# Kernel tuning notes

Hardware: AMD Instinct MI355X
Metric: run time of the kernel (lower is better)

## Reference

```python
import jax, jax.numpy as jnp
import numpy as np

B, H, W, C = 32, 64, 64, 512
NH, WIN, SHIFT = 16, 8, 4
S = WIN * WIN           # tokens per window = 64
HD = C // NH            # head dim = 32
FF = 4 * C
EPS = 1e-5
NW = (H // WIN) * (W // WIN)  # windows per image = 64


def _build_attn_mask():
    # Static shifted-window mask, same construction as SwinBlock_tp.__init__
    img = np.zeros((H, W), np.float32)
    slices = (slice(0, -WIN), slice(-WIN, -SHIFT), slice(-SHIFT, None))
    cnt = 0
    for hs in slices:
        for ws in slices:
            img[hs, ws] = cnt
            cnt += 1
    # window_partition on (1,H,W,1)
    m = img.reshape(H // WIN, WIN, W // WIN, WIN).transpose(0, 2, 1, 3).reshape(-1, S)
    diff = m[:, None, :] - m[:, :, None]            # (NW, S, S)
    return jnp.asarray(diff != 0)[:, None, :, :]     # (NW, 1, S, S) bool, True = masked

_ATTN_MASK = _build_attn_mask()


def _layernorm(x, g, b):
    mu = jnp.mean(x, axis=-1, keepdims=True)
    var = jnp.var(x, axis=-1, keepdims=True)
    return (x - mu) * jax.lax.rsqrt(var + EPS) * g + b


def _window_partition(x):
    # (B,H,W,C) -> (B*NW, S, C)
    x = x.reshape(B, H // WIN, WIN, W // WIN, WIN, C)
    x = x.transpose(0, 1, 3, 2, 4, 5)
    return x.reshape(-1, S, C)


def _window_reverse(x):
    # (B*NW, S, C) -> (B,H,W,C)
    x = x.reshape(B, H // WIN, W // WIN, WIN, WIN, C)
    x = x.transpose(0, 1, 3, 2, 4, 5)
    return x.reshape(B, H, W, C)


def setup_inputs() -> dict:
    key = jax.random.key(0)
    ks = jax.random.split(key, 8)
    sd = 0.02
    return {
        "hidden_states": jax.random.normal(ks[0], (B, H * W, C), jnp.float32),
        "Wqkv": jax.random.normal(ks[1], (C, 3 * C), jnp.float32) * sd,
        "bqkv": jnp.zeros((3 * C,), jnp.float32),
        "Wo": jax.random.normal(ks[2], (C, C), jnp.float32) * sd,
        "bo": jnp.zeros((C,), jnp.float32),
        "ln1_g": jnp.ones((C,), jnp.float32),
        "ln1_b": jnp.zeros((C,), jnp.float32),
        "ln2_g": jnp.ones((C,), jnp.float32),
        "ln2_b": jnp.zeros((C,), jnp.float32),
        "W1": jax.random.normal(ks[3], (C, FF), jnp.float32) * sd,
        "b1": jnp.zeros((FF,), jnp.float32),
        "W2": jax.random.normal(ks[4], (FF, C), jnp.float32) * sd,
        "b2": jnp.zeros((C,), jnp.float32),
    }


def reference(hidden_states, Wqkv, bqkv, Wo, bo, ln1_g, ln1_b, ln2_g, ln2_b, W1, b1, W2, b2):
    shortcut = hidden_states
    x = _layernorm(hidden_states, ln1_g, ln1_b).reshape(B, H, W, C)
    x = jnp.roll(x, shift=(-SHIFT, -SHIFT), axis=(1, 2))
    xw = _window_partition(x)                                  # (B*NW, S, C)

    qkv = xw @ Wqkv + bqkv                                     # (B*NW, S, 3C)
    q, k, v = jnp.split(qkv, 3, axis=-1)
    q = q.reshape(-1, S, NH, HD)
    k = k.reshape(-1, S, NH, HD)
    v = v.reshape(-1, S, NH, HD)
    scale = 1.0 / jnp.sqrt(jnp.float32(HD))
    scores = jnp.einsum("nqhd,nkhd->nhqk", q, k) * scale      # (B*NW, NH, S, S)
    mask = jnp.tile(_ATTN_MASK, (B, 1, 1, 1))                  # (B*NW, 1, S, S)
    scores = jnp.where(mask, -10000.0, scores)
    probs = jax.nn.softmax(scores, axis=-1)
    attn = jnp.einsum("nhqk,nkhd->nqhd", probs, v).reshape(-1, S, C)
    attn = attn @ Wo + bo                                      # out proj (+bias fused)

    x = _window_reverse(attn)
    x = jnp.roll(x, shift=(SHIFT, SHIFT), axis=(1, 2)).reshape(B, H * W, C)
    x = shortcut + x

    y = _layernorm(x, ln2_g, ln2_b)
    y = jax.nn.gelu(y @ W1 + b1, approximate=True) @ W2 + b2
    return x + y
```

## Files before the change

kernel.cpp:

```cpp
#include <hip/hip_runtime.h>
#include <hip/hip_bf16.h>
#include <math.h>

typedef __bf16 bf16_t;
typedef __bf16 bf16x8 __attribute__((ext_vector_type(8)));
typedef float  f32x4  __attribute__((ext_vector_type(4)));

__device__ __forceinline__ int inputs_f32(const unsigned* disc) {
  return disc[0] != 0x3F803F80u;
}

__device__ __forceinline__ float load1(const void* p, size_t i, int f32) {
  return f32 ? ((const float*)p)[i] : (float)((const bf16_t*)p)[i];
}

__device__ __forceinline__ void load_lds16(const bf16_t* g, bf16_t* l) {
  __builtin_amdgcn_global_load_lds(
      (const __attribute__((address_space(1))) void*)g,
      (__attribute__((address_space(3))) void*)l, 16, 0, 0);
}

__device__ __forceinline__ int region_of(int wh, int ww, int s) {
  int i = s >> 3, j = s & 7;
  int h = wh * 8 + i, w = ww * 8 + j;
  int rh = (h < 56) ? 0 : (h < 60 ? 1 : 2);
  int rw = (w < 56) ? 0 : (w < 60 ? 1 : 2);
  return rh * 3 + rw;
}

__global__ __launch_bounds__(256) void transpose_cvt(const void* __restrict__ in,
                                                     bf16_t* __restrict__ out, int R, int C,
                                                     const unsigned* __restrict__ disc) {
  int f32 = inputs_f32(disc);
  __shared__ bf16_t tile[32][33];
  int tc = blockIdx.x * 32, tr = blockIdx.y * 32;
  int tx = threadIdx.x & 31, ty = threadIdx.x >> 5;
  for (int rr = ty; rr < 32; rr += 8)
    tile[rr][tx] = (bf16_t)load1(in, (size_t)(tr + rr) * C + tc + tx, f32);
  __syncthreads();
  for (int rr = ty; rr < 32; rr += 8)
    out[(size_t)(tc + rr) * R + tr + tx] = tile[tx][rr];
}

__global__ void cvt_vec(const void* __restrict__ src, bf16_t* __restrict__ dst, int n,
                        const unsigned* __restrict__ disc) {
  int f32 = inputs_f32(disc);
  int i = blockIdx.x * 256 + threadIdx.x;
  if (i < n) dst[i] = (bf16_t)load1(src, i, f32);
}

template<int PERM>
__global__ __launch_bounds__(256) void ln_kernel(const void* __restrict__ x,
                                                 const bf16_t* __restrict__ g,
                                                 const bf16_t* __restrict__ b,
                                                 bf16_t* __restrict__ out,
                                                 int row0,
                                                 const unsigned* __restrict__ disc) {
  int f32 = PERM ? inputs_f32(disc) : 0;
  int wave = threadIdx.x >> 6, lane = threadIdx.x & 63;
  int r = blockIdx.x * 4 + wave;
  size_t srcrow;
  if (PERM) {
    int bi = r >> 12, nw = (r >> 6) & 63, s = r & 63;
    int wh = nw >> 3, ww = nw & 7, ii = s >> 3, jj = s & 7;
    int h = (wh * 8 + ii + 4) & 63, w = (ww * 8 + jj + 4) & 63;
    srcrow = (size_t)row0 + ((bi << 12) | (h << 6) | w);
  } else {
    srcrow = (size_t)r;
  }
  float f[8];
  if (f32) {
    const float* fp = (const float*)x + srcrow * 512 + lane * 8;
    float4 a = ((const float4*)fp)[0], c = ((const float4*)fp)[1];
    f[0]=a.x; f[1]=a.y; f[2]=a.z; f[3]=a.w; f[4]=c.x; f[5]=c.y; f[6]=c.z; f[7]=c.w;
  } else {
    bf16x8 v = *(const bf16x8*)((const bf16_t*)x + srcrow * 512 + lane * 8);
#pragma unroll
    for (int k = 0; k < 8; ++k) f[k] = (float)v[k];
  }
  float sum = 0.f;
#pragma unroll
  for (int k = 0; k < 8; ++k) sum += f[k];
#pragma unroll
  for (int off = 1; off < 64; off <<= 1) sum += __shfl_xor(sum, off);
  float mu = sum * (1.0f / 512.0f);
  float sq = 0.f;
#pragma unroll
  for (int k = 0; k < 8; ++k) { float d = f[k] - mu; sq += d * d; }
#pragma unroll
  for (int off = 1; off < 64; off <<= 1) sq += __shfl_xor(sq, off);
  float rstd = rsqrtf(sq * (1.0f / 512.0f) + 1e-5f);
  bf16x8 gv = *(const bf16x8*)(g + lane * 8);
  bf16x8 bv = *(const bf16x8*)(b + lane * 8);
  bf16x8 ov;
#pragma unroll
  for (int k = 0; k < 8; ++k)
    ov[k] = (bf16_t)((f[k] - mu) * rstd * (float)gv[k] + (float)bv[k]);
  *(bf16x8*)(out + (size_t)r * 512 + lane * 8) = ov;
}

__device__ __forceinline__ float gelu_f(float x) {
  float t = tanhf(0.7978845608028654f * (x + 0.044715f * x * x * x));
  return 0.5f * x * (1.0f + t);
}

template<int MODE>
__global__ __launch_bounds__(256) void gemm_bt(const bf16_t* __restrict__ A,
                                               const bf16_t* __restrict__ Bt,
                                               const bf16_t* __restrict__ bias,
                                               const void* extra_raw,
                                               const bf16_t* extra_bf,
                                               void* out_raw,
                                               bf16_t* out_bf,
                                               int row0,
                                               const unsigned* __restrict__ disc,
                                               int N, int K) {
  int f32 = (MODE == 1 || MODE == 3) ? inputs_f32(disc) : 0;
  __shared__ __align__(16) bf16_t As[128 * 32];
  __shared__ __align__(16) bf16_t Bs[128 * 32];
  int ntiles = N >> 7;
  int mtile = blockIdx.x / ntiles, ntile = blockIdx.x % ntiles;
  int tid = threadIdx.x, lane = tid & 63, wave = tid >> 6;
  int moff = (wave >> 1) * 64, noff = (wave & 1) * 64;
  int quad = lane >> 4, l15 = lane & 15;
  const bf16_t* Ab = A + (size_t)mtile * 128 * K;
  const bf16_t* Bb = Bt + (size_t)ntile * 128 * K;

  f32x4 acc[4][4] = {};
  for (int k0 = 0; k0 < K; k0 += 32) {
#pragma unroll
    for (int cc = 0; cc < 2; ++cc) {
      int c = tid + cc * 256;
      int row = c >> 2, ko = (c & 3) * 8;
      bf16_t* lA = As + (size_t)(wave * 64 + cc * 256) * 8;
      bf16_t* lB = Bs + (size_t)(wave * 64 + cc * 256) * 8;
      const bf16_t* gsrc = Ab + (size_t)row * K + k0 + ko;
      const bf16_t* gsrcB = Bb + (size_t)row * K + k0 + ko;
      load_lds16(gsrc, lA);
      load_lds16(gsrcB, lB);
    }
    __syncthreads();
    bf16x8 af[4], bff[4];
#pragma unroll
    for (int t = 0; t < 4; ++t) {
      af[t]  = *(const bf16x8*)(As + (moff + t * 16 + l15) * 32 + quad * 8);
      bff[t] = *(const bf16x8*)(Bs + (noff + t * 16 + l15) * 32 + quad * 8);
    }
#pragma unroll
    for (int mt = 0; mt < 4; ++mt)
#pragma unroll
      for (int nt = 0; nt < 4; ++nt)
        acc[mt][nt] = __builtin_amdgcn_mfma_f32_16x16x32_bf16(af[mt], bff[nt], acc[mt][nt], 0, 0, 0);
    __syncthreads();
  }
#pragma unroll
  for (int mt = 0; mt < 4; ++mt) {
#pragma unroll
    for (int nt = 0; nt < 4; ++nt) {
      int gn = (ntile << 7) + noff + nt * 16 + l15;
      float bi = (float)bias[gn];
#pragma unroll
      for (int i = 0; i < 4; ++i) {
        int gm = (mtile << 7) + moff + mt * 16 + quad * 4 + i;
        float v = acc[mt][nt][i] + bi;
        if (MODE == 2) v = gelu_f(v);
        if (MODE == 0 || MODE == 2) {
          out_bf[(size_t)gm * N + gn] = (bf16_t)v;
        } else if (MODE == 1) {
          int bimg = gm >> 12, nw = (gm >> 6) & 63, s = gm & 63;
          int wh = nw >> 3, ww = nw & 7, ii = s >> 3, jj = s & 7;
          int h = (wh * 8 + ii + 4) & 63, w = (ww * 8 + jj + 4) & 63;
          int t = (bimg << 12) | (h << 6) | w;
          v += load1(extra_raw, ((size_t)row0 + t) * 512 + gn, f32);
          out_bf[(size_t)t * 512 + gn] = (bf16_t)v;
        } else {
          v += (float)extra_bf[(size_t)gm * 512 + gn];
          size_t oidx = ((size_t)row0 + gm) * 512 + gn;
          if (f32) ((float*)out_raw)[oidx] = v;
          else     ((bf16_t*)out_raw)[oidx] = (bf16_t)v;
        }
      }
    }
  }
}

__global__ __launch_bounds__(64) void attn_scalar(const bf16_t* __restrict__ qkv,
                                                  bf16_t* __restrict__ attn_out) {
  __shared__ float Ks[64][33];
  __shared__ float Vs[64][33];
  int win = blockIdx.x >> 4, head = blockIdx.x & 15;
  int nw = win & 63, wh = nw >> 3, ww = nw & 7;
  const bf16_t* base = qkv + (size_t)win * 64 * 1536 + head * 32;
  int t = threadIdx.x;
  const bf16_t* krow = base + 512 + (size_t)t * 1536;
  const bf16_t* vrow = base + 1024 + (size_t)t * 1536;
#pragma unroll
  for (int d = 0; d < 32; ++d) { Ks[t][d] = (float)krow[d]; Vs[t][d] = (float)vrow[d]; }
  __syncthreads();

  float q[32];
  const bf16_t* qrow = base + (size_t)t * 1536;
#pragma unroll
  for (int d = 0; d < 32; ++d) q[d] = (float)qrow[d];

  const float scale = 0.17677669529663687f;
  int rr = region_of(wh, ww, t);
  float sc[64];
  float mx = -1e30f;
#pragma unroll
  for (int k = 0; k < 64; ++k) {
    float s = 0.f;
#pragma unroll
    for (int d = 0; d < 32; ++d) s += q[d] * Ks[k][d];
    s *= scale;
    if (region_of(wh, ww, k) != rr) s = -10000.0f;
    sc[k] = s;
    mx = fmaxf(mx, s);
  }
  float sum = 0.f;
#pragma unroll
  for (int k = 0; k < 64; ++k) { sc[k] = __expf(sc[k] - mx); sum += sc[k]; }
  float inv = 1.0f / sum;
  float o[32];
#pragma unroll
  for (int d = 0; d < 32; ++d) o[d] = 0.f;
#pragma unroll
  for (int k = 0; k < 64; ++k) {
    float p = sc[k] * inv;
#pragma unroll
    for (int d = 0; d < 32; ++d) o[d] += p * Vs[k][d];
  }
  bf16_t* orow = attn_out + (size_t)win * 64 * 512 + (size_t)t * 512 + head * 32;
#pragma unroll
  for (int d = 0; d < 32; ++d) orow[d] = (bf16_t)o[d];
}

extern "C" void kernel_launch(void* const* d_in, const int* in_sizes, int n_in,
                              void* d_out, int out_size, void* d_ws, size_t ws_size,
                              hipStream_t stream) {
  (void)in_sizes; (void)n_in; (void)out_size; (void)ws_size;
  const void* hidden = d_in[0];
  const void* Wqkv = d_in[1];  const void* bqkv = d_in[2];
  const void* Wo   = d_in[3];  const void* bo   = d_in[4];
  const void* ln1g = d_in[5];  const void* ln1b = d_in[6];
  const void* ln2g = d_in[7];  const void* ln2b = d_in[8];
  const void* W1   = d_in[9];  const void* b1   = d_in[10];
  const void* W2   = d_in[11]; const void* b2   = d_in[12];
  const unsigned* disc = (const unsigned*)d_in[5];
  char* ws = (char*)d_ws;

  bf16_t* WqkvT = (bf16_t*)ws;
  bf16_t* WoT   = WqkvT + 1536 * 512;
  bf16_t* W1T   = WoT + 512 * 512;
  bf16_t* W2T   = W1T + 2048 * 512;
  bf16_t* cbqkv = W2T + 2048 * 512;
  bf16_t* cbo   = cbqkv + 1536;
  bf16_t* cb1   = cbo + 512;
  bf16_t* cb2   = cb1 + 2048;
  bf16_t* cl1g  = cb2 + 512;
  bf16_t* cl1b  = cl1g + 512;
  bf16_t* cl2g  = cl1b + 512;
  bf16_t* cl2b  = cl2g + 512;
  bf16_t* R1 = (bf16_t*)(ws + 0x00800000ULL);
  bf16_t* R2 = (bf16_t*)(ws + 0x02800000ULL);
  bf16_t* R3 = (bf16_t*)(ws + 0x0A800000ULL);
  bf16_t* R4 = (bf16_t*)(ws + 0x0C800000ULL);

  transpose_cvt<<<dim3(48, 16), 256, 0, stream>>>(Wqkv, WqkvT, 512, 1536, disc);
  transpose_cvt<<<dim3(16, 16), 256, 0, stream>>>(Wo, WoT, 512, 512, disc);
  transpose_cvt<<<dim3(64, 16), 256, 0, stream>>>(W1, W1T, 512, 2048, disc);
  transpose_cvt<<<dim3(16, 64), 256, 0, stream>>>(W2, W2T, 2048, 512, disc);
  cvt_vec<<<6, 256, 0, stream>>>(bqkv, cbqkv, 1536, disc);
  cvt_vec<<<2, 256, 0, stream>>>(bo, cbo, 512, disc);
  cvt_vec<<<8, 256, 0, stream>>>(b1, cb1, 2048, disc);
  cvt_vec<<<2, 256, 0, stream>>>(b2, cb2, 512, disc);
  cvt_vec<<<2, 256, 0, stream>>>(ln1g, cl1g, 512, disc);
  cvt_vec<<<2, 256, 0, stream>>>(ln1b, cl1b, 512, disc);
  cvt_vec<<<2, 256, 0, stream>>>(ln2g, cl2g, 512, disc);
  cvt_vec<<<2, 256, 0, stream>>>(ln2b, cl2b, 512, disc);

  for (int c = 0; c < 4; ++c) {
    int row0 = c * 32768;
    bf16_t* xw    = R1;
    bf16_t* qkvc  = R2;
    bf16_t* attnO = R1;
    bf16_t* xresc = R3;
    bf16_t* xln2c = R4;
    bf16_t* ffnh  = R2;
    ln_kernel<1><<<8192, 256, 0, stream>>>(hidden, cl1g, cl1b, xw, row0, disc);
    gemm_bt<0><<<3072, 256, 0, stream>>>(xw, WqkvT, cbqkv, nullptr, nullptr, nullptr, qkvc,
                                         0, disc, 1536, 512);
    attn_scalar<<<8192, 64, 0, stream>>>(qkvc, attnO);
    gemm_bt<1><<<1024, 256, 0, stream>>>(attnO, WoT, cbo, hidden, nullptr, nullptr, xresc,
                                         row0, disc, 512, 512);
    ln_kernel<0><<<8192, 256, 0, stream>>>(xresc, cl2g, cl2b, xln2c, 0, disc);
    gemm_bt<2><<<4096, 256, 0, stream>>>(xln2c, W1T, cb1, nullptr, nullptr, nullptr, ffnh,
                                         0, disc, 2048, 512);
    gemm_bt<3><<<1024, 256, 0, stream>>>(ffnh, W2T, cb2, nullptr, xresc, d_out, nullptr,
                                         row0, disc, 512, 2048);
  }
}
```

Baseline: 2.894 ms.

## Double-buffer GEMM LDS tiles, swizzle block order, vectorize attention loads/stores

Double-buffers the GEMM's A/B LDS tiles so the global-to-LDS loads for the next K-slice are issued before the MFMAs on the current slice, leaving one barrier per iteration. Remaps block indices with a stride-8 swizzle, presumably to spread consecutive blocks across XCDs or improve L2 locality. In the scalar attention kernel, q/k/v loads and output stores become 16-byte bf16x8 vector accesses instead of per-element ones. Doubles LDS use per block, which may lower occupancy, and the swizzle assumes the grid size is divisible by 8.

```diff
diff --git a/kernel.cpp b/kernel.cpp
--- a/kernel.cpp
+++ b/kernel.cpp
@@ -116,35 +116,43 @@
                                                const unsigned* __restrict__ disc,
                                                int N, int K) {
   int f32 = (MODE == 1 || MODE == 3) ? inputs_f32(disc) : 0;
-  __shared__ __align__(16) bf16_t As[128 * 32];
-  __shared__ __align__(16) bf16_t Bs[128 * 32];
+  __shared__ __align__(16) bf16_t As[2 * 128 * 32];
+  __shared__ __align__(16) bf16_t Bs[2 * 128 * 32];
   int ntiles = N >> 7;
-  int mtile = blockIdx.x / ntiles, ntile = blockIdx.x % ntiles;
+  int cpx = gridDim.x >> 3;
+  int swz = ((int)blockIdx.x & 7) * cpx + ((int)blockIdx.x >> 3);
+  int mtile = swz / ntiles, ntile = swz % ntiles;
   int tid = threadIdx.x, lane = tid & 63, wave = tid >> 6;
   int moff = (wave >> 1) * 64, noff = (wave & 1) * 64;
   int quad = lane >> 4, l15 = lane & 15;
   const bf16_t* Ab = A + (size_t)mtile * 128 * K;
   const bf16_t* Bb = Bt + (size_t)ntile * 128 * K;
 
-  f32x4 acc[4][4] = {};
-  for (int k0 = 0; k0 < K; k0 += 32) {
+  auto stage = [&](int buf, int k0) {
 #pragma unroll
     for (int cc = 0; cc < 2; ++cc) {
       int c = tid + cc * 256;
       int row = c >> 2, ko = (c & 3) * 8;
-      bf16_t* lA = As + (size_t)(wave * 64 + cc * 256) * 8;
-      bf16_t* lB = Bs + (size_t)(wave * 64 + cc * 256) * 8;
-      const bf16_t* gsrc = Ab + (size_t)row * K + k0 + ko;
-      const bf16_t* gsrcB = Bb + (size_t)row * K + k0 + ko;
-      load_lds16(gsrc, lA);
-      load_lds16(gsrcB, lB);
+      bf16_t* lA = As + buf * 4096 + (size_t)(wave * 64 + cc * 256) * 8;
+      bf16_t* lB = Bs + buf * 4096 + (size_t)(wave * 64 + cc * 256) * 8;
+      load_lds16(Ab + (size_t)row * K + k0 + ko, lA);
+      load_lds16(Bb + (size_t)row * K + k0 + ko, lB);
     }
-    __syncthreads();
+  };
+
+  f32x4 acc[4][4] = {};
+  stage(0, 0);
+  __syncthreads();
+  int cur = 0;
+  for (int k0 = 0; k0 < K; k0 += 32) {
+    if (k0 + 32 < K) stage(cur ^ 1, k0 + 32);
+    const bf16_t* Ac = As + cur * 4096;
+    const bf16_t* Bc = Bs + cur * 4096;
     bf16x8 af[4], bff[4];
 #pragma unroll
     for (int t = 0; t < 4; ++t) {
-      af[t]  = *(const bf16x8*)(As + (moff + t * 16 + l15) * 32 + quad * 8);
-      bff[t] = *(const bf16x8*)(Bs + (noff + t * 16 + l15) * 32 + quad * 8);
+      af[t]  = *(const bf16x8*)(Ac + (moff + t * 16 + l15) * 32 + quad * 8);
+      bff[t] = *(const bf16x8*)(Bc + (noff + t * 16 + l15) * 32 + quad * 8);
     }
 #pragma unroll
     for (int mt = 0; mt < 4; ++mt)
@@ -152,6 +160,7 @@
       for (int nt = 0; nt < 4; ++nt)
         acc[mt][nt] = __builtin_amdgcn_mfma_f32_16x16x32_bf16(af[mt], bff[nt], acc[mt][nt], 0, 0, 0);
     __syncthreads();
+    cur ^= 1;
   }
 #pragma unroll
   for (int mt = 0; mt < 4; ++mt) {
@@ -195,13 +204,22 @@
   const bf16_t* krow = base + 512 + (size_t)t * 1536;
   const bf16_t* vrow = base + 1024 + (size_t)t * 1536;
 #pragma unroll
-  for (int d = 0; d < 32; ++d) { Ks[t][d] = (float)krow[d]; Vs[t][d] = (float)vrow[d]; }
+  for (int i = 0; i < 4; ++i) {
+    bf16x8 kv = *(const bf16x8*)(krow + i * 8);
+    bf16x8 vv = *(const bf16x8*)(vrow + i * 8);
+#pragma unroll
+    for (int j = 0; j < 8; ++j) { Ks[t][i * 8 + j] = (float)kv[j]; Vs[t][i * 8 + j] = (float)vv[j]; }
+  }
   __syncthreads();
 
   float q[32];
   const bf16_t* qrow = base + (size_t)t * 1536;
 #pragma unroll
-  for (int d = 0; d < 32; ++d) q[d] = (float)qrow[d];
+  for (int i = 0; i < 4; ++i) {
+    bf16x8 qv = *(const bf16x8*)(qrow + i * 8);
+#pragma unroll
+    for (int j = 0; j < 8; ++j) q[i * 8 + j] = (float)qv[j];
+  }
 
   const float scale = 0.17677669529663687f;
   int rr = region_of(wh, ww, t);
@@ -232,7 +250,12 @@
   }
   bf16_t* orow = attn_out + (size_t)win * 64 * 512 + (size_t)t * 512 + head * 32;
 #pragma unroll
-  for (int d = 0; d < 32; ++d) orow[d] = (bf16_t)o[d];
+  for (int i = 0; i < 4; ++i) {
+    bf16x8 ov;
+#pragma unroll
+    for (int j = 0; j < 8; ++j) ov[j] = (bf16_t)o[i * 8 + j];
+    *(bf16x8*)(orow + i * 8) = ov;
+  }
 }
 
 extern "C" void kernel_launch(void* const* d_in, const int* in_sizes, int n_in,
```

Result: faster. 2.749 ms (-5.0%).
